# Optimization experiments

Hardware: AMD Instinct MI355X
Metric: run time of the kernel (lower is better)

The kernel has to match this reference:

```python
import jax, jax.numpy as jnp
import numpy as np
from jax import lax

WIN = 11
NUM_CLASSES = 2
WEIGHTS = (1.0, 0.5)
PAD = (WIN - 1) // 2


def _edge_kernel():
    w = -jnp.ones((1, 1, WIN, WIN), jnp.float32)
    return w.at[0, 0, WIN // 2, WIN // 2].set(WIN * WIN - 1.0)


def setup_inputs() -> dict:
    key = jax.random.key(0)
    k0, k1, k2 = jax.random.split(key, 3)
    B, H, W = 16, 1024, 1024
    score0 = jax.random.normal(k0, (B, NUM_CLASSES, H, W), jnp.float32)
    score1 = jax.random.normal(k1, (B, NUM_CLASSES, H, W), jnp.float32)
    target = jax.random.randint(k2, (B, 1, H, W), 0, NUM_CLASSES, jnp.int32)
    return {"score0": score0, "score1": score1, "target": target}


def _loss_one(x, onehot, edge_mask, smoothing):
    # x: [B,C,H,W] logits; onehot: [B,C,H,W]; edge_mask: [B,1,H,W]
    log_p = jax.nn.log_softmax(x, axis=1)
    alpha = smoothing
    # softlabel: filled with alpha, target class gets 1 - alpha + alpha/C
    soft = alpha + onehot * (1.0 - 2.0 * alpha + alpha / NUM_CLASSES)
    mask = onehot * (1.0 - edge_mask) + soft * edge_mask
    # sum over class dim, mean over (B,H,W), negated
    return -jnp.mean(jnp.sum(mask * log_p, axis=1))


def reference(score0, score1, target):
    tgt_f = target.astype(jnp.float32)  # [B,1,H,W]
    edge = lax.conv_general_dilated(
        tgt_f, _edge_kernel(), window_strides=(1, 1),
        padding=((PAD, PAD), (PAD, PAD)),
        dimension_numbers=("NCHW", "OIHW", "NCHW"))
    edge_mask = (edge != 0).astype(jnp.float32)          # [B,1,H,W]
    smoothing = jnp.minimum(jnp.mean(edge_mask), 0.2)
    cls = jnp.arange(NUM_CLASSES, dtype=jnp.int32).reshape(1, NUM_CLASSES, 1, 1)
    onehot = (target == cls).astype(jnp.float32)         # [B,C,H,W]
    loss = (WEIGHTS[0] * _loss_one(score0, onehot, edge_mask, smoothing)
            + WEIGHTS[1] * _loss_one(score1, onehot, edge_mask, smoothing))
    return loss
```

## Files before the change

### kernel.cpp

```cpp
#include <hip/hip_runtime.h>

#define TW   128
#define TH   32
#define HALO 5
#define TIW  (TW + 2*HALO)
#define TIH  (TH + 2*HALO)
#define TB_P 144
#define VS_P 142
#define NBX  8
#define NBY  32
#define NBZ  16
#define NB   (NBX*NBY*NBZ)
#define NPIX 16777216.0

__global__ __launch_bounds__(256)
void fused_edge_loss(const float* __restrict__ score0,
                     const float* __restrict__ score1,
                     const int*   __restrict__ target,
                     float*       __restrict__ ws) {
    __shared__ unsigned char  tb[TIH][TB_P];
    __shared__ unsigned short vs[TH][VS_P];
    __shared__ float          red[4][5];

    const int tid   = threadIdx.x;
    const int tileX = blockIdx.x * TW;
    const int tileY = blockIdx.y * TH;
    const int b     = blockIdx.z;
    const int bid   = (blockIdx.z * NBY + blockIdx.y) * NBX + blockIdx.x;

    const int* tgt = target + (size_t)b * (1024 * 1024);

    for (int idx = tid; idx < TIH * TIW; idx += 256) {
        int rr = idx / TIW;
        int cc = idx - rr * TIW;
        int gr = tileY + rr - HALO;
        int gc = tileX + cc - HALO;
        unsigned char v = 0;
        if ((unsigned)gr < 1024u && (unsigned)gc < 1024u)
            v = (unsigned char)tgt[gr * 1024 + gc];
        tb[rr][cc] = v;
    }
    __syncthreads();

    if (tid < TIW) {
        int acc = 0;
        #pragma unroll
        for (int rr = 0; rr < 11; ++rr) acc += tb[rr][tid];
        vs[0][tid] = (unsigned short)acc;
        for (int r = 1; r < TH; ++r) {
            acc += (int)tb[r + 10][tid] - (int)tb[r - 1][tid];
            vs[r][tid] = (unsigned short)acc;
        }
    }
    __syncthreads();

    const float* s0b = score0 + (size_t)b * (2 * 1024 * 1024);
    const float* s1b = score1 + (size_t)b * (2 * 1024 * 1024);
    const int tx = tid & 31;
    const int ty = tid >> 5;

    float cnt = 0.f, a1 = 0.f, a2 = 0.f, b1 = 0.f, b2 = 0.f;

    #pragma unroll
    for (int p = 0; p < 4; ++p) {
        const int r  = ty + p * 8;
        const int gr = tileY + r;
        const int c0 = tx * 4;
        const int gc = tileX + c0;

        int S[4];
        int s = 0;
        #pragma unroll
        for (int k = 0; k < 11; ++k) s += vs[r][c0 + k];
        S[0] = s;
        #pragma unroll
        for (int j = 1; j < 4; ++j) {
            s += (int)vs[r][c0 + 10 + j] - (int)vs[r][c0 + j - 1];
            S[j] = s;
        }

        const size_t base = (size_t)gr * 1024 + gc;
        float4 x0 = *(const float4*)(s0b + base);
        float4 x1 = *(const float4*)(s0b + 1048576 + base);
        float4 y0 = *(const float4*)(s1b + base);
        float4 y1 = *(const float4*)(s1b + 1048576 + base);
        float p0a[4] = {x0.x, x0.y, x0.z, x0.w};
        float p1a[4] = {x1.x, x1.y, x1.z, x1.w};
        float q0a[4] = {y0.x, y0.y, y0.z, y0.w};
        float q1a[4] = {y1.x, y1.y, y1.z, y1.w};

        #pragma unroll
        for (int j = 0; j < 4; ++j) {
            const int t = tb[r + 5][c0 + 5 + j];
            const float e = (S[j] != 121 * t) ? 1.0f : 0.0f;
            cnt += e;

            {
                float p0 = p0a[j], p1 = p1a[j];
                float m   = fmaxf(p0, p1);
                float lse = m + __logf(1.0f + __expf(-fabsf(p0 - p1)));
                float lpt = (t ? p1 : p0) - lse;
                float slp = p0 + p1 - 2.0f * lse;
                a1 += lpt;
                a2 += e * (slp - 1.5f * lpt);
            }
            {
                float q0 = q0a[j], q1 = q1a[j];
                float m   = fmaxf(q0, q1);
                float lse = m + __logf(1.0f + __expf(-fabsf(q0 - q1)));
                float lpt = (t ? q1 : q0) - lse;
                float slp = q0 + q1 - 2.0f * lse;
                b1 += lpt;
                b2 += e * (slp - 1.5f * lpt);
            }
        }
    }

    float vals[5] = {cnt, a1, a2, b1, b2};
    const int lane = tid & 63, wv = tid >> 6;
    #pragma unroll
    for (int q = 0; q < 5; ++q) {
        float v = vals[q];
        #pragma unroll
        for (int off = 32; off > 0; off >>= 1) v += __shfl_down(v, off);
        if (lane == 0) red[wv][q] = v;
    }
    __syncthreads();
    if (tid == 0) {
        #pragma unroll
        for (int q = 0; q < 5; ++q) {
            float v = red[0][q] + red[1][q] + red[2][q] + red[3][q];
            ws[q * NB + bid] = v;
        }
    }
}

__global__ __launch_bounds__(256)
void finalize_loss(const float* __restrict__ ws, float* __restrict__ out) {
    __shared__ double red[4][5];
    const int tid = threadIdx.x;
    double acc[5] = {0, 0, 0, 0, 0};
    for (int i = tid; i < NB; i += 256) {
        #pragma unroll
        for (int q = 0; q < 5; ++q) acc[q] += (double)ws[q * NB + i];
    }
    const int lane = tid & 63, wv = tid >> 6;
    #pragma unroll
    for (int q = 0; q < 5; ++q) {
        double v = acc[q];
        #pragma unroll
        for (int off = 32; off > 0; off >>= 1) v += __shfl_down(v, off);
        if (lane == 0) red[wv][q] = v;
    }
    __syncthreads();
    if (tid == 0) {
        double s[5];
        #pragma unroll
        for (int q = 0; q < 5; ++q)
            s[q] = red[0][q] + red[1][q] + red[2][q] + red[3][q];
        const double N = NPIX;
        double alpha = s[0] / N;
        if (alpha > 0.2) alpha = 0.2;
        double loss = (s[1] + alpha * s[2]) + 0.5 * (s[3] + alpha * s[4]);
        out[0] = (float)(-loss / N);
    }
}

extern "C" void kernel_launch(void* const* d_in, const int* in_sizes, int n_in,
                              void* d_out, int out_size, void* d_ws, size_t ws_size,
                              hipStream_t stream) {
    const float* score0 = (const float*)d_in[0];
    const float* score1 = (const float*)d_in[1];
    const int*   target = (const int*)d_in[2];
    float* out = (float*)d_out;
    float* ws  = (float*)d_ws;

    dim3 grid(NBX, NBY, NBZ);
    fused_edge_loss<<<grid, 256, 0, stream>>>(score0, score1, target, ws);
    finalize_loss<<<1, 256, 0, stream>>>(ws, out);
}
```

Measured before the change: 341.4 us.

## Split edge mask into a byte-code prepass and a flat streaming loss kernel

Splits the fused kernel into two. The first computes the per-pixel target and edge bit from the 11x11 box sum and writes one byte per pixel to workspace. The second is a flat grid-stride style kernel that streams score0/score1 with float4 loads and reads the byte code, with no shared-memory tile setup. This removes the halo loads and box-sum work from the bandwidth-bound pass. In exchange it adds a 16 MB write and read of the code buffer and an extra launch. The old fused path is kept as a fallback when the workspace is too small.

```diff
diff --git a/kernel.cpp b/kernel.cpp
--- a/kernel.cpp
+++ b/kernel.cpp
@@ -13,20 +13,18 @@
 #define NB   (NBX*NBY*NBZ)
 #define NPIX 16777216.0
 
+#define CODE_BYTES (16u*1024u*1024u)
+#define NB2 4096
+
 __global__ __launch_bounds__(256)
-void fused_edge_loss(const float* __restrict__ score0,
-                     const float* __restrict__ score1,
-                     const int*   __restrict__ target,
-                     float*       __restrict__ ws) {
+void edge_code(const int* __restrict__ target, unsigned char* __restrict__ code) {
     __shared__ unsigned char  tb[TIH][TB_P];
     __shared__ unsigned short vs[TH][VS_P];
-    __shared__ float          red[4][5];
 
     const int tid   = threadIdx.x;
     const int tileX = blockIdx.x * TW;
     const int tileY = blockIdx.y * TH;
     const int b     = blockIdx.z;
-    const int bid   = (blockIdx.z * NBY + blockIdx.y) * NBX + blockIdx.x;
 
     const int* tgt = target + (size_t)b * (1024 * 1024);
 
@@ -54,6 +52,168 @@
     }
     __syncthreads();
 
+    const int tx = tid & 31;
+    const int ty = tid >> 5;
+    unsigned char* cb = code + (size_t)b * (1024 * 1024);
+
+    #pragma unroll
+    for (int p = 0; p < 4; ++p) {
+        const int r  = ty + p * 8;
+        const int gr = tileY + r;
+        const int c0 = tx * 4;
+        const int gc = tileX + c0;
+
+        int S[4];
+        int s = 0;
+        #pragma unroll
+        for (int k = 0; k < 11; ++k) s += vs[r][c0 + k];
+        S[0] = s;
+        #pragma unroll
+        for (int j = 1; j < 4; ++j) {
+            s += (int)vs[r][c0 + 10 + j] - (int)vs[r][c0 + j - 1];
+            S[j] = s;
+        }
+
+        unsigned int w = 0;
+        #pragma unroll
+        for (int j = 0; j < 4; ++j) {
+            const int t = tb[r + 5][c0 + 5 + j];
+            const unsigned int e = (S[j] != 121 * t) ? 1u : 0u;
+            w |= (((unsigned int)t) | (e << 1)) << (8 * j);
+        }
+        *(unsigned int*)(cb + (size_t)gr * 1024 + gc) = w;
+    }
+}
+
+__device__ __forceinline__ void proc4(unsigned int cw,
+                                      float4 x0, float4 x1, float4 y0, float4 y1,
+                                      float& cnt, float& a1, float& a2,
+                                      float& b1, float& b2) {
+    float p0a[4] = {x0.x, x0.y, x0.z, x0.w};
+    float p1a[4] = {x1.x, x1.y, x1.z, x1.w};
+    float q0a[4] = {y0.x, y0.y, y0.z, y0.w};
+    float q1a[4] = {y1.x, y1.y, y1.z, y1.w};
+    #pragma unroll
+    for (int j = 0; j < 4; ++j) {
+        const unsigned int cbyte = (cw >> (8 * j)) & 0xffu;
+        const int   t = (int)(cbyte & 1u);
+        const float e = (float)((cbyte >> 1) & 1u);
+        cnt += e;
+        {
+            float p0 = p0a[j], p1 = p1a[j];
+            float m   = fmaxf(p0, p1);
+            float lse = m + __logf(1.0f + __expf(-fabsf(p0 - p1)));
+            float lpt = (t ? p1 : p0) - lse;
+            float slp = p0 + p1 - 2.0f * lse;
+            a1 += lpt;
+            a2 += e * (slp - 1.5f * lpt);
+        }
+        {
+            float q0 = q0a[j], q1 = q1a[j];
+            float m   = fmaxf(q0, q1);
+            float lse = m + __logf(1.0f + __expf(-fabsf(q0 - q1)));
+            float lpt = (t ? q1 : q0) - lse;
+            float slp = q0 + q1 - 2.0f * lse;
+            b1 += lpt;
+            b2 += e * (slp - 1.5f * lpt);
+        }
+    }
+}
+
+__global__ __launch_bounds__(256)
+void loss_stream(const float* __restrict__ score0,
+                 const float* __restrict__ score1,
+                 const unsigned char* __restrict__ code,
+                 float* __restrict__ partials) {
+    __shared__ float red[4][5];
+    const int tid = threadIdx.x;
+    const int bid = blockIdx.x;
+
+    const size_t P0 = 4u * (size_t)(bid * 256 + tid);
+    const int    b0 = (int)(P0 >> 20);
+    const size_t rr = P0 & 1048575u;
+    const float* s0p = score0 + (size_t)b0 * 2097152u + rr;
+    const float* s1p = score1 + (size_t)b0 * 2097152u + rr;
+    const unsigned int* cp = (const unsigned int*)(code + P0);
+
+    float cnt = 0.f, a1 = 0.f, a2 = 0.f, b1 = 0.f, b2 = 0.f;
+
+    #pragma unroll
+    for (int i = 0; i < 4; i += 2) {
+        const size_t fA = (size_t)i       * 8388608u;
+        const size_t fB = (size_t)(i + 1) * 8388608u;
+        const unsigned int cwA = cp[(size_t)i       * 1048576u];
+        const unsigned int cwB = cp[(size_t)(i + 1) * 1048576u];
+        float4 xA0 = *(const float4*)(s0p + fA);
+        float4 xA1 = *(const float4*)(s0p + fA + 1048576u);
+        float4 yA0 = *(const float4*)(s1p + fA);
+        float4 yA1 = *(const float4*)(s1p + fA + 1048576u);
+        float4 xB0 = *(const float4*)(s0p + fB);
+        float4 xB1 = *(const float4*)(s0p + fB + 1048576u);
+        float4 yB0 = *(const float4*)(s1p + fB);
+        float4 yB1 = *(const float4*)(s1p + fB + 1048576u);
+        proc4(cwA, xA0, xA1, yA0, yA1, cnt, a1, a2, b1, b2);
+        proc4(cwB, xB0, xB1, yB0, yB1, cnt, a1, a2, b1, b2);
+    }
+
+    float vals[5] = {cnt, a1, a2, b1, b2};
+    const int lane = tid & 63, wv = tid >> 6;
+    #pragma unroll
+    for (int q = 0; q < 5; ++q) {
+        float v = vals[q];
+        #pragma unroll
+        for (int off = 32; off > 0; off >>= 1) v += __shfl_down(v, off);
+        if (lane == 0) red[wv][q] = v;
+    }
+    __syncthreads();
+    if (tid == 0) {
+        #pragma unroll
+        for (int q = 0; q < 5; ++q)
+            partials[q * NB2 + bid] = red[0][q] + red[1][q] + red[2][q] + red[3][q];
+    }
+}
+
+__global__ __launch_bounds__(256)
+void fused_edge_loss(const float* __restrict__ score0,
+                     const float* __restrict__ score1,
+                     const int*   __restrict__ target,
+                     float*       __restrict__ ws) {
+    __shared__ unsigned char  tb[TIH][TB_P];
+    __shared__ unsigned short vs[TH][VS_P];
+    __shared__ float          red[4][5];
+
+    const int tid   = threadIdx.x;
+    const int tileX = blockIdx.x * TW;
+    const int tileY = blockIdx.y * TH;
+    const int b     = blockIdx.z;
+    const int bid   = (blockIdx.z * NBY + blockIdx.y) * NBX + blockIdx.x;
+
+    const int* tgt = target + (size_t)b * (1024 * 1024);
+
+    for (int idx = tid; idx < TIH * TIW; idx += 256) {
+        int rr = idx / TIW;
+        int cc = idx - rr * TIW;
+        int gr = tileY + rr - HALO;
+        int gc = tileX + cc - HALO;
+        unsigned char v = 0;
+        if ((unsigned)gr < 1024u && (unsigned)gc < 1024u)
+            v = (unsigned char)tgt[gr * 1024 + gc];
+        tb[rr][cc] = v;
+    }
+    __syncthreads();
+
+    if (tid < TIW) {
+        int acc = 0;
+        #pragma unroll
+        for (int rr = 0; rr < 11; ++rr) acc += tb[rr][tid];
+        vs[0][tid] = (unsigned short)acc;
+        for (int r = 1; r < TH; ++r) {
+            acc += (int)tb[r + 10][tid] - (int)tb[r - 1][tid];
+            vs[r][tid] = (unsigned short)acc;
+        }
+    }
+    __syncthreads();
+
     const float* s0b = score0 + (size_t)b * (2 * 1024 * 1024);
     const float* s1b = score1 + (size_t)b * (2 * 1024 * 1024);
     const int tx = tid & 31;
@@ -94,7 +254,6 @@
             const int t = tb[r + 5][c0 + 5 + j];
             const float e = (S[j] != 121 * t) ? 1.0f : 0.0f;
             cnt += e;
-
             {
                 float p0 = p0a[j], p1 = p1a[j];
                 float m   = fmaxf(p0, p1);
@@ -173,9 +332,20 @@
     const float* score1 = (const float*)d_in[1];
     const int*   target = (const int*)d_in[2];
     float* out = (float*)d_out;
-    float* ws  = (float*)d_ws;
-
-    dim3 grid(NBX, NBY, NBZ);
-    fused_edge_loss<<<grid, 256, 0, stream>>>(score0, score1, target, ws);
-    finalize_loss<<<1, 256, 0, stream>>>(ws, out);
-}
+    unsigned char* ws = (unsigned char*)d_ws;
+
+    const size_t need = (size_t)CODE_BYTES + (size_t)5 * NB2 * 4;
+    if (ws_size >= need) {
+        unsigned char* code     = ws;
+        float*         partials = (float*)(ws + CODE_BYTES);
+        dim3 g1(NBX, NBY, NBZ);
+        edge_code<<<g1, 256, 0, stream>>>(target, code);
+        loss_stream<<<NB2, 256, 0, stream>>>(score0, score1, code, partials);
+        finalize_loss<<<1, 256, 0, stream>>>(partials, out);
+    } else {
+        float* partials = (float*)ws;
+        dim3 grid(NBX, NBY, NBZ);
+        fused_edge_loss<<<grid, 256, 0, stream>>>(score0, score1, target, partials);
+        finalize_loss<<<1, 256, 0, stream>>>(partials, out);
+    }
+}
```

Measured after the change: 346.7 us. No clear change (+1.6%).

## Bit-pack targets and compute edge mask via bitwise OR/AND morphology

Applied to the files above, without the earlier changes.

Adds a pipeline in which the int32 target is packed into 1-bit-per-pixel words with wave ballots. An 11x11 min/max (OR/AND) over the bits then yields the edge mask, since for binary targets the Laplacian is nonzero exactly when the window is not uniform. A flat streaming loss kernel then reads the scores with float4 loads and the bitmasks. This replaces the shared-memory box-sum tiling and its halo reloads, at the cost of two extra small kernel launches and extra workspace. The new path only holds for binary targets and falls back to the old fused kernel when the workspace is too small.

```diff
diff --git a/kernel.cpp b/kernel.cpp
--- a/kernel.cpp
+++ b/kernel.cpp
@@ -1,4 +1,14 @@
 #include <hip/hip_runtime.h>
+
+typedef float v2f __attribute__((ext_vector_type(2)));
+typedef unsigned long long u64;
+
+#define NPIX 16777216.0
+
+#define TBITS_OFF 0u
+#define EBITS_OFF (2u*1024u*1024u)
+#define PART_OFF  (4u*1024u*1024u)
+#define NB2       8192
 
 #define TW   128
 #define TH   32
@@ -11,7 +21,220 @@
 #define NBY  32
 #define NBZ  16
 #define NB   (NBX*NBY*NBZ)
-#define NPIX 16777216.0
+
+__global__ __launch_bounds__(256)
+void pack_bits(const int* __restrict__ target, u64* __restrict__ tbits) {
+    const int gtid = blockIdx.x * 256 + threadIdx.x;
+    const int wave = gtid >> 6;
+    const int lane = threadIdx.x & 63;
+    #pragma unroll 2
+    for (int i = 0; i < 32; i += 4) {
+        const size_t w = (size_t)wave * 32 + i;
+        const int v0 = target[((w + 0) << 6) | lane];
+        const int v1 = target[((w + 1) << 6) | lane];
+        const int v2 = target[((w + 2) << 6) | lane];
+        const int v3 = target[((w + 3) << 6) | lane];
+        const u64 m0 = __ballot(v0 != 0);
+        const u64 m1 = __ballot(v1 != 0);
+        const u64 m2 = __ballot(v2 != 0);
+        const u64 m3 = __ballot(v3 != 0);
+        if (lane == 0) {
+            tbits[w + 0] = m0;
+            tbits[w + 1] = m1;
+            tbits[w + 2] = m2;
+            tbits[w + 3] = m3;
+        }
+    }
+}
+
+__device__ __forceinline__ u64 hor11_or(u64 L, u64 M, u64 R) {
+    u64 o = M;
+    o |= (M >> 1) | (R << 63);
+    o |= (M >> 2) | (R << 62);
+    o |= (M >> 3) | (R << 61);
+    o |= (M >> 4) | (R << 60);
+    o |= (M >> 5) | (R << 59);
+    o |= (M << 1) | (L >> 63);
+    o |= (M << 2) | (L >> 62);
+    o |= (M << 3) | (L >> 61);
+    o |= (M << 4) | (L >> 60);
+    o |= (M << 5) | (L >> 59);
+    return o;
+}
+__device__ __forceinline__ u64 hor11_and(u64 L, u64 M, u64 R) {
+    u64 a = M;
+    a &= (M >> 1) | (R << 63);
+    a &= (M >> 2) | (R << 62);
+    a &= (M >> 3) | (R << 61);
+    a &= (M >> 4) | (R << 60);
+    a &= (M >> 5) | (R << 59);
+    a &= (M << 1) | (L >> 63);
+    a &= (M << 2) | (L >> 62);
+    a &= (M << 3) | (L >> 61);
+    a &= (M << 4) | (L >> 60);
+    a &= (M << 5) | (L >> 59);
+    return a;
+}
+
+__global__ __launch_bounds__(256)
+void edge_bits(const u64* __restrict__ tbits, u64* __restrict__ ebits) {
+    const int idx = blockIdx.x * 256 + threadIdx.x;
+    const int wi  = idx & 15;
+    const int row = (idx >> 4) & 1023;
+    const int b   = idx >> 14;
+    const u64* plane = tbits + (size_t)b * 16384;
+
+    u64 oL = 0, oM = 0, oR = 0;
+    u64 aL = ~0ull, aM = ~0ull, aR = ~0ull;
+    #pragma unroll
+    for (int dr = -5; dr <= 5; ++dr) {
+        const int r = row + dr;
+        u64 L = 0, M = 0, R = 0;
+        if ((unsigned)r < 1024u) {
+            const u64* rp = plane + (size_t)r * 16;
+            L = (wi > 0)  ? rp[wi - 1] : 0ull;
+            M = rp[wi];
+            R = (wi < 15) ? rp[wi + 1] : 0ull;
+        }
+        oL |= L; oM |= M; oR |= R;
+        aL &= L; aM &= M; aR &= R;
+    }
+    const u64 O = hor11_or(oL, oM, oR);
+    const u64 A = hor11_and(aL, aM, aR);
+    ebits[idx] = O ^ A;
+}
+
+__device__ __forceinline__ void acc_pair(v2f p0, v2f p1, unsigned t0, unsigned t1,
+                                         v2f ef, v2f& s1, v2f& s2) {
+    v2f d = p0 - p1;
+    v2f sp;
+    sp.x = __logf(1.0f + __expf(-fabsf(d.x)));
+    sp.y = __logf(1.0f + __expf(-fabsf(d.y)));
+    v2f m;
+    m.x = fmaxf(p0.x, p1.x);
+    m.y = fmaxf(p0.y, p1.y);
+    v2f lse = m + sp;
+    v2f pt;
+    pt.x = t0 ? p1.x : p0.x;
+    pt.y = t1 ? p1.y : p0.y;
+    v2f lpt = pt - lse;
+    v2f slp = (p0 + p1) - 2.0f * lse;
+    s1 += lpt;
+    s2 += ef * (slp - 1.5f * lpt);
+}
+
+__device__ __forceinline__ void proc_group(float4 x0, float4 x1, float4 y0, float4 y1,
+                                           unsigned nt, unsigned ne,
+                                           v2f& cntv, v2f& a1, v2f& a2, v2f& b1, v2f& b2) {
+    #pragma unroll
+    for (int h = 0; h < 2; ++h) {
+        const unsigned t0 = (nt >> (2 * h)) & 1u;
+        const unsigned t1 = (nt >> (2 * h + 1)) & 1u;
+        const unsigned e0 = (ne >> (2 * h)) & 1u;
+        const unsigned e1 = (ne >> (2 * h + 1)) & 1u;
+        v2f ef; ef.x = (float)e0; ef.y = (float)e1;
+        cntv += ef;
+        v2f p0, p1, q0, q1;
+        p0.x = h ? x0.z : x0.x;  p0.y = h ? x0.w : x0.y;
+        p1.x = h ? x1.z : x1.x;  p1.y = h ? x1.w : x1.y;
+        q0.x = h ? y0.z : y0.x;  q0.y = h ? y0.w : y0.y;
+        q1.x = h ? y1.z : y1.x;  q1.y = h ? y1.w : y1.y;
+        acc_pair(p0, p1, t0, t1, ef, a1, a2);
+        acc_pair(q0, q1, t0, t1, ef, b1, b2);
+    }
+}
+
+__global__ __launch_bounds__(256)
+void loss_stream2(const float* __restrict__ score0,
+                  const float* __restrict__ score1,
+                  const unsigned int* __restrict__ tb32,
+                  const unsigned int* __restrict__ eb32,
+                  float* __restrict__ partials) {
+    __shared__ float red[4][5];
+    const int tid = threadIdx.x;
+    const int bid = blockIdx.x;
+    const int g   = bid * 256 + tid;
+
+    const size_t PA = 4ull * (size_t)g;
+    const size_t PB = PA + 8388608ull;
+
+    const float* pA0 = score0 + (PA >> 20) * 2097152u + (PA & 1048575u);
+    const float* pA1 = score1 + (PA >> 20) * 2097152u + (PA & 1048575u);
+    const float* pB0 = score0 + (PB >> 20) * 2097152u + (PB & 1048575u);
+    const float* pB1 = score1 + (PB >> 20) * 2097152u + (PB & 1048575u);
+
+    const float4 xA0 = *(const float4*)(pA0);
+    const float4 xA1 = *(const float4*)(pA0 + 1048576);
+    const float4 yA0 = *(const float4*)(pA1);
+    const float4 yA1 = *(const float4*)(pA1 + 1048576);
+    const float4 xB0 = *(const float4*)(pB0);
+    const float4 xB1 = *(const float4*)(pB0 + 1048576);
+    const float4 yB0 = *(const float4*)(pB1);
+    const float4 yB1 = *(const float4*)(pB1 + 1048576);
+    const unsigned twA = tb32[PA >> 5], ewA = eb32[PA >> 5];
+    const unsigned twB = tb32[PB >> 5], ewB = eb32[PB >> 5];
+
+    const unsigned shA = (unsigned)PA & 31u;
+    const unsigned shB = (unsigned)PB & 31u;
+    const unsigned ntA = (twA >> shA) & 15u, neA = (ewA >> shA) & 15u;
+    const unsigned ntB = (twB >> shB) & 15u, neB = (ewB >> shB) & 15u;
+
+    v2f cntv = {0.f, 0.f}, a1 = {0.f, 0.f}, a2 = {0.f, 0.f};
+    v2f b1 = {0.f, 0.f}, b2 = {0.f, 0.f};
+    proc_group(xA0, xA1, yA0, yA1, ntA, neA, cntv, a1, a2, b1, b2);
+    proc_group(xB0, xB1, yB0, yB1, ntB, neB, cntv, a1, a2, b1, b2);
+
+    float vals[5] = {cntv.x + cntv.y, a1.x + a1.y, a2.x + a2.y,
+                     b1.x + b1.y, b2.x + b2.y};
+    const int lane = tid & 63, wv = tid >> 6;
+    #pragma unroll
+    for (int q = 0; q < 5; ++q) {
+        float v = vals[q];
+        #pragma unroll
+        for (int off = 32; off > 0; off >>= 1) v += __shfl_down(v, off);
+        if (lane == 0) red[wv][q] = v;
+    }
+    __syncthreads();
+    if (tid == 0) {
+        #pragma unroll
+        for (int q = 0; q < 5; ++q)
+            partials[q * NB2 + bid] = red[0][q] + red[1][q] + red[2][q] + red[3][q];
+    }
+}
+
+__global__ __launch_bounds__(1024)
+void finalize_loss(const float* __restrict__ ws, float* __restrict__ out, int n) {
+    __shared__ double red[16][5];
+    const int tid = threadIdx.x;
+    double acc[5] = {0, 0, 0, 0, 0};
+    for (int i = tid; i < n; i += 1024) {
+        #pragma unroll
+        for (int q = 0; q < 5; ++q) acc[q] += (double)ws[q * n + i];
+    }
+    const int lane = tid & 63, wv = tid >> 6;
+    #pragma unroll
+    for (int q = 0; q < 5; ++q) {
+        double v = acc[q];
+        #pragma unroll
+        for (int off = 32; off > 0; off >>= 1) v += __shfl_down(v, off);
+        if (lane == 0) red[wv][q] = v;
+    }
+    __syncthreads();
+    if (tid == 0) {
+        double s[5];
+        #pragma unroll
+        for (int q = 0; q < 5; ++q) {
+            double v = 0;
+            for (int w = 0; w < 16; ++w) v += red[w][q];
+            s[q] = v;
+        }
+        const double N = NPIX;
+        double alpha = s[0] / N;
+        if (alpha > 0.2) alpha = 0.2;
+        double loss = (s[1] + alpha * s[2]) + 0.5 * (s[3] + alpha * s[4]);
+        out[0] = (float)(-loss / N);
+    }
+}
 
 __global__ __launch_bounds__(256)
 void fused_edge_loss(const float* __restrict__ score0,
@@ -94,7 +317,6 @@
             const int t = tb[r + 5][c0 + 5 + j];
             const float e = (S[j] != 121 * t) ? 1.0f : 0.0f;
             cnt += e;
-
             {
                 float p0 = p0a[j], p1 = p1a[j];
                 float m   = fmaxf(p0, p1);
@@ -135,37 +357,6 @@
     }
 }
 
-__global__ __launch_bounds__(256)
-void finalize_loss(const float* __restrict__ ws, float* __restrict__ out) {
-    __shared__ double red[4][5];
-    const int tid = threadIdx.x;
-    double acc[5] = {0, 0, 0, 0, 0};
-    for (int i = tid; i < NB; i += 256) {
-        #pragma unroll
-        for (int q = 0; q < 5; ++q) acc[q] += (double)ws[q * NB + i];
-    }
-    const int lane = tid & 63, wv = tid >> 6;
-    #pragma unroll
-    for (int q = 0; q < 5; ++q) {
-        double v = acc[q];
-        #pragma unroll
-        for (int off = 32; off > 0; off >>= 1) v += __shfl_down(v, off);
-        if (lane == 0) red[wv][q] = v;
-    }
-    __syncthreads();
-    if (tid == 0) {
-        double s[5];
-        #pragma unroll
-        for (int q = 0; q < 5; ++q)
-            s[q] = red[0][q] + red[1][q] + red[2][q] + red[3][q];
-        const double N = NPIX;
-        double alpha = s[0] / N;
-        if (alpha > 0.2) alpha = 0.2;
-        double loss = (s[1] + alpha * s[2]) + 0.5 * (s[3] + alpha * s[4]);
-        out[0] = (float)(-loss / N);
-    }
-}
-
 extern "C" void kernel_launch(void* const* d_in, const int* in_sizes, int n_in,
                               void* d_out, int out_size, void* d_ws, size_t ws_size,
                               hipStream_t stream) {
@@ -173,9 +364,23 @@
     const float* score1 = (const float*)d_in[1];
     const int*   target = (const int*)d_in[2];
     float* out = (float*)d_out;
-    float* ws  = (float*)d_ws;
-
-    dim3 grid(NBX, NBY, NBZ);
-    fused_edge_loss<<<grid, 256, 0, stream>>>(score0, score1, target, ws);
-    finalize_loss<<<1, 256, 0, stream>>>(ws, out);
-}
+    unsigned char* ws = (unsigned char*)d_ws;
+
+    const size_t need = (size_t)PART_OFF + (size_t)5 * NB2 * 4;
+    if (ws_size >= need) {
+        u64* tb = (u64*)(ws + TBITS_OFF);
+        u64* eb = (u64*)(ws + EBITS_OFF);
+        float* partials = (float*)(ws + PART_OFF);
+        pack_bits<<<2048, 256, 0, stream>>>(target, tb);
+        edge_bits<<<1024, 256, 0, stream>>>(tb, eb);
+        loss_stream2<<<NB2, 256, 0, stream>>>(score0, score1,
+                                              (const unsigned int*)tb,
+                                              (const unsigned int*)eb, partials);
+        finalize_loss<<<1, 1024, 0, stream>>>(partials, out, NB2);
+    } else {
+        float* partials = (float*)ws;
+        dim3 grid(NBX, NBY, NBZ);
+        fused_edge_loss<<<grid, 256, 0, stream>>>(score0, score1, target, partials);
+        finalize_loss<<<1, 1024, 0, stream>>>(partials, out, NB);
+    }
+}
```

Result: faster. 330.9 us (-3.1%).
